# Kernel tuning notes

Hardware: AMD Instinct MI355X
Metric: run time of the kernel (lower is better)

## Reference

```python
import jax, jax.numpy as jnp
import numpy as np

D_MODEL = 1024
NUM_HEADS = 16
HEAD_DIM = D_MODEL // NUM_HEADS
B, S = 4, 2048


def setup_inputs() -> dict:
    key = jax.random.key(0)
    ks = jax.random.split(key, 12)
    s = 1.0 / np.sqrt(D_MODEL)
    return {
        "inputs_q": jax.random.normal(ks[0], (B, S, D_MODEL), jnp.float32),
        "inputs_k": jax.random.normal(ks[1], (B, S, D_MODEL), jnp.float32),
        "inputs_v": jax.random.normal(ks[2], (B, S, D_MODEL), jnp.float32),
        "Wq": jax.random.normal(ks[3], (D_MODEL, D_MODEL), jnp.float32) * s,
        "bq": jax.random.normal(ks[4], (D_MODEL,), jnp.float32) * 0.01,
        "Wk": jax.random.normal(ks[5], (D_MODEL, D_MODEL), jnp.float32) * s,
        "bk": jax.random.normal(ks[6], (D_MODEL,), jnp.float32) * 0.01,
        "Wv": jax.random.normal(ks[7], (D_MODEL, D_MODEL), jnp.float32) * s,
        "bv": jax.random.normal(ks[8], (D_MODEL,), jnp.float32) * 0.01,
        "Wo": jax.random.normal(ks[9], (D_MODEL, D_MODEL), jnp.float32) * s,
        "bo": jax.random.normal(ks[10], (D_MODEL,), jnp.float32) * 0.01,
    }


def reference(inputs_q, inputs_k, inputs_v, Wq, bq, Wk, bk, Wv, bv, Wo, bo):
    b, s, _ = inputs_q.shape
    # linear projections
    q = inputs_q @ Wq + bq  # [b, s, d_model]
    k = inputs_k @ Wk + bk
    v = inputs_v @ Wv + bv
    # split heads: bsd -> bhsd
    q = q.reshape(b, s, NUM_HEADS, HEAD_DIM).transpose(0, 2, 1, 3)
    k = k.reshape(b, s, NUM_HEADS, HEAD_DIM).transpose(0, 2, 1, 3)
    v = v.reshape(b, s, NUM_HEADS, HEAD_DIM).transpose(0, 2, 1, 3)
    scale = 1.0 / jnp.sqrt(jnp.asarray(HEAD_DIM, q.dtype))
    scores = jnp.einsum('bhqd,bhkd->bhqk', q, k) * scale  # [b,h,s,s]
    # causal mask: position q attends to k <= q
    causal = jnp.tril(jnp.ones((s, s), dtype=bool))
    scores = jnp.where(causal[None, None], scores, jnp.asarray(-jnp.inf, scores.dtype))
    attn = jax.nn.softmax(scores, axis=-1)
    ctx = jnp.einsum('bhqk,bhkd->bhqd', attn, v)  # [b,h,s,hd]
    ctx = ctx.transpose(0, 2, 1, 3).reshape(b, s, D_MODEL)
    return ctx @ Wo + bo
```

## Files before the change

kernel.cpp:

```cpp
#include <hip/hip_runtime.h>
#include <math.h>
#include <type_traits>

typedef __bf16 bf16;
typedef __attribute__((ext_vector_type(8))) __bf16 bf16x8;
typedef __attribute__((ext_vector_type(4))) float f32x4;
typedef __attribute__((ext_vector_type(16))) float f32x16;

#define SEQ 2048
#define DM 1024
#define NH 16
#define HD 64
#define BATCH 4

#define NEG_BIG (-1e30f)
#define SCALE_L2E 0.18033688011f

__device__ inline bf16x8 cvt_f32x8(const float* p) {
  f32x4 x0 = *(const f32x4*)p;
  f32x4 x1 = *(const f32x4*)(p + 4);
  bf16x8 r;
  r[0] = (bf16)x0[0]; r[1] = (bf16)x0[1]; r[2] = (bf16)x0[2]; r[3] = (bf16)x0[3];
  r[4] = (bf16)x1[0]; r[5] = (bf16)x1[1]; r[6] = (bf16)x1[2]; r[7] = (bf16)x1[3];
  return r;
}

__device__ inline void async_copy16(const bf16* g, bf16* l) {
  __builtin_amdgcn_global_load_lds(
      (const __attribute__((address_space(1))) unsigned int*)g,
      (__attribute__((address_space(3))) unsigned int*)l, 16, 0, 0);
}

__global__ __launch_bounds__(256) void cvt_kernel(const float* __restrict__ src,
                                                  bf16* __restrict__ dst) {
  size_t i = ((size_t)blockIdx.x * 256 + threadIdx.x) * 8;
  *(bf16x8*)(dst + i) = cvt_f32x8(src + i);
}

__global__ __launch_bounds__(256) void transpose_w_kernel(
    const float* __restrict__ Wq, const float* __restrict__ Wk,
    const float* __restrict__ Wv, const float* __restrict__ Wo,
    bf16* __restrict__ Tq, bf16* __restrict__ Tk,
    bf16* __restrict__ Tv, bf16* __restrict__ To) {
  __shared__ bf16 tile[64 * 66];
  int z = blockIdx.z;
  const float* src = (z == 0) ? Wq : (z == 1) ? Wk : (z == 2) ? Wv : Wo;
  bf16* dst = (z == 0) ? Tq : (z == 1) ? Tk : (z == 2) ? Tv : To;
  int n0 = blockIdx.x * 64, k0 = blockIdx.y * 64;
  int t = threadIdx.x;
  int c = t & 63, rr = t >> 6;
#pragma unroll
  for (int i = 0; i < 16; i++) {
    int k = i * 4 + rr;
    tile[k * 66 + c] = (bf16)src[(size_t)(k0 + k) * DM + n0 + c];
  }
  __syncthreads();
#pragma unroll
  for (int i = 0; i < 16; i++) {
    int n = i * 4 + rr;
    dst[(size_t)(n0 + n) * DM + k0 + c] = tile[c * 66 + n];
  }
}

__global__ __launch_bounds__(256) void transpose_v_kernel(
    const bf16* __restrict__ Vc, bf16* __restrict__ Vt) {
  __shared__ bf16 tile[64 * 66];
  int s0 = blockIdx.x * 64;
  int bh = blockIdx.y;
  int t = threadIdx.x;
  int c = t & 63, rr = t >> 6;
  const bf16* src = Vc + (size_t)bh * SEQ * HD;
  bf16* dst = Vt + (size_t)bh * HD * SEQ;
#pragma unroll
  for (int i = 0; i < 16; i++) {
    int s = i * 4 + rr;
    tile[s * 66 + c] = src[(size_t)(s0 + s) * HD + c];
  }
  __syncthreads();
#pragma unroll
  for (int i = 0; i < 16; i++) {
    int d = i * 4 + rr;
    dst[(size_t)d * SEQ + s0 + c] = tile[c * 66 + d];
  }
}

template <typename CT, int MODE>
__global__ __launch_bounds__(256) void gemm_bias_kernel(
    const bf16* __restrict__ A, const bf16* __restrict__ Bt,
    const float* __restrict__ bias, CT* __restrict__ C) {
  __shared__ bf16 As[128 * 32];
  __shared__ bf16 Bs[128 * 32];
  int m0 = blockIdx.x * 128, n0 = blockIdx.y * 128;
  int t = threadIdx.x;
  int wave = t >> 6, lane = t & 63, lr = lane & 15, lq = lane >> 4;
  int wm = (wave & 1) * 64, wn = (wave >> 1) * 64;

  f32x4 acc[4][4];
#pragma unroll
  for (int i = 0; i < 4; i++)
#pragma unroll
    for (int j = 0; j < 4; j++) acc[i][j] = (f32x4){0.f, 0.f, 0.f, 0.f};

  int srow = wave * 32 + (lane >> 2);
  int skc = lane & 3;
  const bf16* gA0 = A + (size_t)(m0 + srow) * DM + skc * 8;
  const bf16* gA1 = gA0 + (size_t)16 * DM;
  const bf16* gB0 = Bt + (size_t)(n0 + srow) * DM + skc * 8;
  const bf16* gB1 = gB0 + (size_t)16 * DM;
  bf16* lA0 = &As[(wave * 128) * 8];
  bf16* lA1 = &As[(wave * 128 + 64) * 8];
  bf16* lB0 = &Bs[(wave * 128) * 8];
  bf16* lB1 = &Bs[(wave * 128 + 64) * 8];

  for (int k0 = 0; k0 < DM; k0 += 32) {
    async_copy16(gA0, lA0);
    async_copy16(gA1, lA1);
    async_copy16(gB0, lB0);
    async_copy16(gB1, lB1);
    gA0 += 32; gA1 += 32; gB0 += 32; gB1 += 32;
    __syncthreads();

    bf16x8 af[4], bfr[4];
#pragma unroll
    for (int i = 0; i < 4; i++)
      af[i] = *(const bf16x8*)&As[(wm + i * 16 + lr) * 32 + lq * 8];
#pragma unroll
    for (int j = 0; j < 4; j++)
      bfr[j] = *(const bf16x8*)&Bs[(wn + j * 16 + lr) * 32 + lq * 8];
#pragma unroll
    for (int i = 0; i < 4; i++)
#pragma unroll
      for (int j = 0; j < 4; j++)
        acc[i][j] = __builtin_amdgcn_mfma_f32_16x16x32_bf16(af[i], bfr[j],
                                                            acc[i][j], 0, 0, 0);
    __syncthreads();
  }

#pragma unroll
  for (int j = 0; j < 4; j++) {
    int col = n0 + wn + j * 16 + lr;
    float bv = bias[col];
#pragma unroll
    for (int i = 0; i < 4; i++) {
      int row0 = m0 + wm + i * 16 + lq * 4;
#pragma unroll
      for (int r = 0; r < 4; r++) {
        int row = row0 + r;
        float v = acc[i][j][r] + bv;
        if constexpr (MODE == 0) {
          C[(size_t)row * DM + col] = (CT)v;
        } else {
          int b = row >> 11, s = row & 2047, h = col >> 6, d = col & 63;
          C[((size_t)(b * NH + h) * SEQ + s) * HD + d] = (CT)v;
        }
      }
    }
  }
}

__attribute__((amdgpu_waves_per_eu(4, 8)))
__global__ __launch_bounds__(256) void attention_kernel(
    const bf16* __restrict__ Qc, const bf16* __restrict__ Kc,
    const bf16* __restrict__ Vt, bf16* __restrict__ ctx) {
  __shared__ float ls_o[2][2][16][64];
  __shared__ float ls_ml[2][2][64];

  int t = threadIdx.x, wave = t >> 6, lane = t & 63;
  int l31 = lane & 31, hh = lane >> 5;
  int pair = wave >> 1, sub = wave & 1;

  int bid = blockIdx.x;
  int xcd = bid & 7, qq = bid >> 3;
  int g = xcd + 8 * (qq & 7);
  int bx = qq >> 3;
  int h = g & 15, b = g >> 4;

  int tq = pair ? (63 - bx) : bx;
  int q0 = tq * 32;
  int nch = tq + 1;
  int half = nch >> 1;
  int c0 = sub ? half : 0;
  int c1 = sub ? nch : half;

  const bf16* Qb = Qc + (size_t)(b * NH + h) * SEQ * HD;
  const bf16* Kb = Kc + (size_t)(b * NH + h) * SEQ * HD;
  const bf16* Vb = Vt + (size_t)(b * NH + h) * HD * SEQ;
  bf16* Cb = ctx + (size_t)b * SEQ * DM + h * HD;

  bf16x8 qf[4];
#pragma unroll
  for (int st = 0; st < 4; st++)
    qf[st] = *(const bf16x8*)&Qb[(size_t)(q0 + l31) * HD + st * 16 + hh * 8];

  f32x16 o[2];
#pragma unroll
  for (int dt = 0; dt < 2; dt++)
#pragma unroll
    for (int r = 0; r < 16; r++) o[dt][r] = 0.f;
  float m_st = NEG_BIG, l_st = 0.f;

#pragma unroll 1
  for (int c = c0; c < c1; c++) {
    int kv0 = c * 32;
    bf16x8 kf[4];
#pragma unroll
    for (int st = 0; st < 4; st++)
      kf[st] = *(const bf16x8*)&Kb[(size_t)(kv0 + l31) * HD + st * 16 + hh * 8];
    bf16x8 vf[2][2];
#pragma unroll
    for (int dt = 0; dt < 2; dt++)
#pragma unroll
      for (int ks = 0; ks < 2; ks++)
        vf[dt][ks] = *(const bf16x8*)&Vb[(size_t)(dt * 32 + l31) * SEQ + kv0 +
                                         ks * 16 + hh * 8];

    f32x16 s;
#pragma unroll
    for (int r = 0; r < 16; r++) s[r] = 0.f;
    __builtin_amdgcn_s_setprio(1);
#pragma unroll
    for (int st = 0; st < 4; st++)
      s = __builtin_amdgcn_mfma_f32_32x32x16_bf16(kf[st], qf[st], s, 0, 0, 0);
    __builtin_amdgcn_s_setprio(0);

    bool diag = (c == nch - 1);
    if (diag) {
      int q_g = q0 + l31;
#pragma unroll
      for (int r = 0; r < 16; r++) {
        int key = kv0 + (r & 3) + 8 * (r >> 2) + 4 * hh;
        float v = s[r] * SCALE_L2E;
        s[r] = (key > q_g) ? NEG_BIG : v;
      }
    } else {
#pragma unroll
      for (int r = 0; r < 16; r++) s[r] *= SCALE_L2E;
    }

    float mx = s[0];
#pragma unroll
    for (int r = 1; r < 16; r++) mx = fmaxf(mx, s[r]);
    mx = fmaxf(mx, __shfl_xor(mx, 32));
    float mnew = fmaxf(m_st, mx);
    float alpha = exp2f(m_st - mnew);
    m_st = mnew;
    float rs = 0.f;
#pragma unroll
    for (int r = 0; r < 16; r++) {
      float pv = exp2f(s[r] - mnew);
      s[r] = pv;
      rs += pv;
    }
    rs += __shfl_xor(rs, 32);
    l_st = l_st * alpha + rs;
#pragma unroll
    for (int dt = 0; dt < 2; dt++)
#pragma unroll
      for (int r = 0; r < 16; r++) o[dt][r] *= alpha;

    unsigned int W[8];
#pragma unroll
    for (int w = 0; w < 8; w++) {
      unsigned int u;
      asm("v_cvt_pk_bf16_f32 %0, %1, %2"
          : "=v"(u)
          : "v"(s[2 * w]), "v"(s[2 * w + 1]));
      W[w] = u;
    }
    bf16x8 pf[2];
    {
      unsigned int x1 = hh ? W[0] : W[2];
      unsigned int x2 = hh ? W[1] : W[3];
      unsigned int x3 = hh ? W[4] : W[6];
      unsigned int x4 = hh ? W[5] : W[7];
      unsigned int y1 = (unsigned int)__shfl_xor((int)x1, 32);
      unsigned int y2 = (unsigned int)__shfl_xor((int)x2, 32);
      unsigned int y3 = (unsigned int)__shfl_xor((int)x3, 32);
      unsigned int y4 = (unsigned int)__shfl_xor((int)x4, 32);
      unsigned int* f0 = (unsigned int*)&pf[0];
      unsigned int* f1 = (unsigned int*)&pf[1];
      f0[0] = hh ? y1 : W[0];
      f0[1] = hh ? y2 : W[1];
      f0[2] = hh ? W[2] : y1;
      f0[3] = hh ? W[3] : y2;
      f1[0] = hh ? y3 : W[4];
      f1[1] = hh ? y4 : W[5];
      f1[2] = hh ? W[6] : y3;
      f1[3] = hh ? W[7] : y4;
    }

    __builtin_amdgcn_s_setprio(1);
#pragma unroll
    for (int dt = 0; dt < 2; dt++)
#pragma unroll
      for (int ks = 0; ks < 2; ks++)
        o[dt] = __builtin_amdgcn_mfma_f32_32x32x16_bf16(vf[dt][ks], pf[ks],
                                                        o[dt], 0, 0, 0);
    __builtin_amdgcn_s_setprio(0);
  }

  if (sub) {
#pragma unroll
    for (int dt = 0; dt < 2; dt++)
#pragma unroll
      for (int r = 0; r < 16; r++) ls_o[pair][dt][r][lane] = o[dt][r];
    ls_ml[pair][0][lane] = m_st;
    ls_ml[pair][1][lane] = l_st;
  }
  __syncthreads();
  if (!sub) {
    float m2 = ls_ml[pair][0][lane], l2 = ls_ml[pair][1][lane];
    float m = fmaxf(m_st, m2);
    float a1 = exp2f(m_st - m), a2 = exp2f(m2 - m);
    float linv = 1.f / (l_st * a1 + l2 * a2);
    int row = q0 + l31;
#pragma unroll
    for (int dt = 0; dt < 2; dt++)
#pragma unroll
      for (int r = 0; r < 16; r += 2) {
        float va = (o[dt][r] * a1 + ls_o[pair][dt][r][lane] * a2) * linv;
        float vb =
            (o[dt][r + 1] * a1 + ls_o[pair][dt][r + 1][lane] * a2) * linv;
        unsigned int u;
        asm("v_cvt_pk_bf16_f32 %0, %1, %2" : "=v"(u) : "v"(va), "v"(vb));
        int d = dt * 32 + (r & 3) + 8 * (r >> 2) + 4 * hh;
        *(unsigned int*)&Cb[(size_t)row * DM + d] = u;
      }
  }
}

extern "C" void kernel_launch(void* const* d_in, const int* in_sizes, int n_in,
                              void* d_out, int out_size, void* d_ws,
                              size_t ws_size, hipStream_t stream) {
  const float* iq = (const float*)d_in[0];
  const float* ik = (const float*)d_in[1];
  const float* iv = (const float*)d_in[2];
  const float* Wq = (const float*)d_in[3];
  const float* bq = (const float*)d_in[4];
  const float* Wk = (const float*)d_in[5];
  const float* bk = (const float*)d_in[6];
  const float* Wv = (const float*)d_in[7];
  const float* bv = (const float*)d_in[8];
  const float* Wo = (const float*)d_in[9];
  const float* bo = (const float*)d_in[10];

  char* ws = (char*)d_ws;
  const size_t MB = 1024 * 1024;
  bf16* Tq = (bf16*)(ws + 0 * MB);
  bf16* Tk = (bf16*)(ws + 2 * MB);
  bf16* Tv = (bf16*)(ws + 4 * MB);
  bf16* To = (bf16*)(ws + 6 * MB);
  bf16* Qc = (bf16*)(ws + 8 * MB);
  bf16* Kc = (bf16*)(ws + 24 * MB);
  bf16* Vc = (bf16*)(ws + 40 * MB);
  bf16* X = (bf16*)d_out;
  bf16* Vtp = (bf16*)d_out;
  bf16* Cx = Vc;

  transpose_w_kernel<<<dim3(16, 16, 4), 256, 0, stream>>>(Wq, Wk, Wv, Wo, Tq,
                                                          Tk, Tv, To);
  cvt_kernel<<<dim3(4096), 256, 0, stream>>>(iq, X);
  gemm_bias_kernel<bf16, 1><<<dim3(64, 8), 256, 0, stream>>>(X, Tq, bq, Qc);
  cvt_kernel<<<dim3(4096), 256, 0, stream>>>(ik, X);
  gemm_bias_kernel<bf16, 1><<<dim3(64, 8), 256, 0, stream>>>(X, Tk, bk, Kc);
  cvt_kernel<<<dim3(4096), 256, 0, stream>>>(iv, X);
  gemm_bias_kernel<bf16, 1><<<dim3(64, 8), 256, 0, stream>>>(X, Tv, bv, Vc);
  transpose_v_kernel<<<dim3(32, 64), 256, 0, stream>>>(Vc, Vtp);
  attention_kernel<<<dim3(2048), 256, 0, stream>>>(Qc, Kc, Vtp, Cx);
  gemm_bias_kernel<float, 0><<<dim3(64, 8), 256, 0, stream>>>(Cx, To, bo,
                                                              (float*)d_out);
}
```

Baseline: 407.6 us.

## Fuse V transpose into projection epilogue and restructure attention work split

The V projection GEMM now writes its output directly in the transposed [b,h,d,s] layout, so the separate transpose kernel and its extra pass over memory go away. The attention kernel drops the split of KV chunks across wave pairs and the LDS merge that recombined them. Each wave now handles two query tiles (one short, one long) in sequence for causal balance, with double-buffered K/V register loads that overlap the next chunk's fetch with the current compute. In exchange, the grid shrinks from 2048 to 512 blocks, the waves_per_eu hint is removed, and the GEMM epilogue does strided stores into the transposed V layout.

```diff
diff --git a/kernel.cpp b/kernel.cpp
--- a/kernel.cpp
+++ b/kernel.cpp
@@ -62,28 +62,6 @@
   }
 }
 
-__global__ __launch_bounds__(256) void transpose_v_kernel(
-    const bf16* __restrict__ Vc, bf16* __restrict__ Vt) {
-  __shared__ bf16 tile[64 * 66];
-  int s0 = blockIdx.x * 64;
-  int bh = blockIdx.y;
-  int t = threadIdx.x;
-  int c = t & 63, rr = t >> 6;
-  const bf16* src = Vc + (size_t)bh * SEQ * HD;
-  bf16* dst = Vt + (size_t)bh * HD * SEQ;
-#pragma unroll
-  for (int i = 0; i < 16; i++) {
-    int s = i * 4 + rr;
-    tile[s * 66 + c] = src[(size_t)(s0 + s) * HD + c];
-  }
-  __syncthreads();
-#pragma unroll
-  for (int i = 0; i < 16; i++) {
-    int d = i * 4 + rr;
-    dst[(size_t)d * SEQ + s0 + c] = tile[c * 66 + d];
-  }
-}
-
 template <typename CT, int MODE>
 __global__ __launch_bounds__(256) void gemm_bias_kernel(
     const bf16* __restrict__ A, const bf16* __restrict__ Bt,
@@ -149,178 +127,174 @@
         float v = acc[i][j][r] + bv;
         if constexpr (MODE == 0) {
           C[(size_t)row * DM + col] = (CT)v;
+        } else if constexpr (MODE == 1) {
+          int b = row >> 11, s = row & 2047, h = col >> 6, d = col & 63;
+          C[((size_t)(b * NH + h) * SEQ + s) * HD + d] = (CT)v;
         } else {
           int b = row >> 11, s = row & 2047, h = col >> 6, d = col & 63;
-          C[((size_t)(b * NH + h) * SEQ + s) * HD + d] = (CT)v;
+          C[((size_t)(b * NH + h) * HD + d) * SEQ + s] = (CT)v;
         }
       }
     }
   }
 }
 
-__attribute__((amdgpu_waves_per_eu(4, 8)))
 __global__ __launch_bounds__(256) void attention_kernel(
     const bf16* __restrict__ Qc, const bf16* __restrict__ Kc,
     const bf16* __restrict__ Vt, bf16* __restrict__ ctx) {
-  __shared__ float ls_o[2][2][16][64];
-  __shared__ float ls_ml[2][2][64];
-
   int t = threadIdx.x, wave = t >> 6, lane = t & 63;
   int l31 = lane & 31, hh = lane >> 5;
-  int pair = wave >> 1, sub = wave & 1;
 
   int bid = blockIdx.x;
   int xcd = bid & 7, qq = bid >> 3;
   int g = xcd + 8 * (qq & 7);
   int bx = qq >> 3;
   int h = g & 15, b = g >> 4;
-
-  int tq = pair ? (63 - bx) : bx;
-  int q0 = tq * 32;
-  int nch = tq + 1;
-  int half = nch >> 1;
-  int c0 = sub ? half : 0;
-  int c1 = sub ? nch : half;
+  int p = bx * 4 + wave;
 
   const bf16* Qb = Qc + (size_t)(b * NH + h) * SEQ * HD;
   const bf16* Kb = Kc + (size_t)(b * NH + h) * SEQ * HD;
   const bf16* Vb = Vt + (size_t)(b * NH + h) * HD * SEQ;
   bf16* Cb = ctx + (size_t)b * SEQ * DM + h * HD;
 
-  bf16x8 qf[4];
-#pragma unroll
-  for (int st = 0; st < 4; st++)
-    qf[st] = *(const bf16x8*)&Qb[(size_t)(q0 + l31) * HD + st * 16 + hh * 8];
-
-  f32x16 o[2];
-#pragma unroll
-  for (int dt = 0; dt < 2; dt++)
-#pragma unroll
-    for (int r = 0; r < 16; r++) o[dt][r] = 0.f;
-  float m_st = NEG_BIG, l_st = 0.f;
-
 #pragma unroll 1
-  for (int c = c0; c < c1; c++) {
-    int kv0 = c * 32;
-    bf16x8 kf[4];
+  for (int pass = 0; pass < 2; pass++) {
+    int tq = pass ? (63 - p) : p;
+    int q0 = tq * 32;
+    int nch = tq + 1;
+    int nch_ev = (nch + 1) & ~1;
+
+    bf16x8 qf[4];
 #pragma unroll
     for (int st = 0; st < 4; st++)
-      kf[st] = *(const bf16x8*)&Kb[(size_t)(kv0 + l31) * HD + st * 16 + hh * 8];
-    bf16x8 vf[2][2];
+      qf[st] = *(const bf16x8*)&Qb[(size_t)(q0 + l31) * HD + st * 16 + hh * 8];
+
+    f32x16 o[2];
 #pragma unroll
     for (int dt = 0; dt < 2; dt++)
 #pragma unroll
-      for (int ks = 0; ks < 2; ks++)
-        vf[dt][ks] = *(const bf16x8*)&Vb[(size_t)(dt * 32 + l31) * SEQ + kv0 +
-                                         ks * 16 + hh * 8];
-
-    f32x16 s;
-#pragma unroll
-    for (int r = 0; r < 16; r++) s[r] = 0.f;
-    __builtin_amdgcn_s_setprio(1);
-#pragma unroll
-    for (int st = 0; st < 4; st++)
-      s = __builtin_amdgcn_mfma_f32_32x32x16_bf16(kf[st], qf[st], s, 0, 0, 0);
-    __builtin_amdgcn_s_setprio(0);
-
-    bool diag = (c == nch - 1);
-    if (diag) {
-      int q_g = q0 + l31;
+      for (int r = 0; r < 16; r++) o[dt][r] = 0.f;
+    float m_st = NEG_BIG, l_st = 0.f;
+
+    bf16x8 kfA[4], vfA[2][2], kfB[4], vfB[2][2];
+
+    auto loadkv = [&](bf16x8(&kf)[4], bf16x8(&vf)[2][2], int c) {
+      int kv0 = c * 32;
+#pragma unroll
+      for (int st = 0; st < 4; st++)
+        kf[st] =
+            *(const bf16x8*)&Kb[(size_t)(kv0 + l31) * HD + st * 16 + hh * 8];
+#pragma unroll
+      for (int dt = 0; dt < 2; dt++)
+#pragma unroll
+        for (int ks = 0; ks < 2; ks++)
+          vf[dt][ks] = *(const bf16x8*)&Vb[(size_t)(dt * 32 + l31) * SEQ + kv0 +
+                                           ks * 16 + hh * 8];
+    };
+
+    auto compute = [&](bf16x8(&kf)[4], bf16x8(&vf)[2][2], int c) {
+      int kv0 = c * 32;
+      f32x16 s;
+#pragma unroll
+      for (int r = 0; r < 16; r++) s[r] = 0.f;
+      __builtin_amdgcn_s_setprio(1);
+#pragma unroll
+      for (int st = 0; st < 4; st++)
+        s = __builtin_amdgcn_mfma_f32_32x32x16_bf16(kf[st], qf[st], s, 0, 0, 0);
+      __builtin_amdgcn_s_setprio(0);
+
+      if (c >= nch - 1) {
+        int q_g = q0 + l31;
+#pragma unroll
+        for (int r = 0; r < 16; r++) {
+          int key = kv0 + (r & 3) + 8 * (r >> 2) + 4 * hh;
+          float v = s[r] * SCALE_L2E;
+          s[r] = (key > q_g) ? NEG_BIG : v;
+        }
+      } else {
+#pragma unroll
+        for (int r = 0; r < 16; r++) s[r] *= SCALE_L2E;
+      }
+
+      float mx = s[0];
+#pragma unroll
+      for (int r = 1; r < 16; r++) mx = fmaxf(mx, s[r]);
+      mx = fmaxf(mx, __shfl_xor(mx, 32));
+      float mnew = fmaxf(m_st, mx);
+      float alpha = exp2f(m_st - mnew);
+      m_st = mnew;
+      float rs = 0.f;
 #pragma unroll
       for (int r = 0; r < 16; r++) {
-        int key = kv0 + (r & 3) + 8 * (r >> 2) + 4 * hh;
-        float v = s[r] * SCALE_L2E;
-        s[r] = (key > q_g) ? NEG_BIG : v;
-      }
-    } else {
-#pragma unroll
-      for (int r = 0; r < 16; r++) s[r] *= SCALE_L2E;
+        float pv = exp2f(s[r] - mnew);
+        s[r] = pv;
+        rs += pv;
+      }
+      rs += __shfl_xor(rs, 32);
+      l_st = l_st * alpha + rs;
+#pragma unroll
+      for (int dt = 0; dt < 2; dt++)
+#pragma unroll
+        for (int r = 0; r < 16; r++) o[dt][r] *= alpha;
+
+      unsigned int W[8];
+#pragma unroll
+      for (int w = 0; w < 8; w++) {
+        unsigned int u;
+        asm("v_cvt_pk_bf16_f32 %0, %1, %2"
+            : "=v"(u)
+            : "v"(s[2 * w]), "v"(s[2 * w + 1]));
+        W[w] = u;
+      }
+      bf16x8 pf[2];
+      {
+        unsigned int x1 = hh ? W[0] : W[2];
+        unsigned int x2 = hh ? W[1] : W[3];
+        unsigned int x3 = hh ? W[4] : W[6];
+        unsigned int x4 = hh ? W[5] : W[7];
+        unsigned int y1 = (unsigned int)__shfl_xor((int)x1, 32);
+        unsigned int y2 = (unsigned int)__shfl_xor((int)x2, 32);
+        unsigned int y3 = (unsigned int)__shfl_xor((int)x3, 32);
+        unsigned int y4 = (unsigned int)__shfl_xor((int)x4, 32);
+        unsigned int* f0 = (unsigned int*)&pf[0];
+        unsigned int* f1 = (unsigned int*)&pf[1];
+        f0[0] = hh ? y1 : W[0];
+        f0[1] = hh ? y2 : W[1];
+        f0[2] = hh ? W[2] : y1;
+        f0[3] = hh ? W[3] : y2;
+        f1[0] = hh ? y3 : W[4];
+        f1[1] = hh ? y4 : W[5];
+        f1[2] = hh ? W[6] : y3;
+        f1[3] = hh ? W[7] : y4;
+      }
+
+      __builtin_amdgcn_s_setprio(1);
+#pragma unroll
+      for (int dt = 0; dt < 2; dt++)
+#pragma unroll
+        for (int ks = 0; ks < 2; ks++)
+          o[dt] = __builtin_amdgcn_mfma_f32_32x32x16_bf16(vf[dt][ks], pf[ks],
+                                                          o[dt], 0, 0, 0);
+      __builtin_amdgcn_s_setprio(0);
+    };
+
+    loadkv(kfA, vfA, 0);
+#pragma unroll 1
+    for (int c = 0; c < nch_ev; c += 2) {
+      loadkv(kfB, vfB, c + 1);
+      compute(kfA, vfA, c);
+      if (c + 2 < nch_ev) loadkv(kfA, vfA, c + 2);
+      compute(kfB, vfB, c + 1);
     }
 
-    float mx = s[0];
-#pragma unroll
-    for (int r = 1; r < 16; r++) mx = fmaxf(mx, s[r]);
-    mx = fmaxf(mx, __shfl_xor(mx, 32));
-    float mnew = fmaxf(m_st, mx);
-    float alpha = exp2f(m_st - mnew);
-    m_st = mnew;
-    float rs = 0.f;
-#pragma unroll
-    for (int r = 0; r < 16; r++) {
-      float pv = exp2f(s[r] - mnew);
-      s[r] = pv;
-      rs += pv;
-    }
-    rs += __shfl_xor(rs, 32);
-    l_st = l_st * alpha + rs;
+    float inv = 1.f / l_st;
+    int row = q0 + l31;
 #pragma unroll
     for (int dt = 0; dt < 2; dt++)
 #pragma unroll
-      for (int r = 0; r < 16; r++) o[dt][r] *= alpha;
-
-    unsigned int W[8];
-#pragma unroll
-    for (int w = 0; w < 8; w++) {
-      unsigned int u;
-      asm("v_cvt_pk_bf16_f32 %0, %1, %2"
-          : "=v"(u)
-          : "v"(s[2 * w]), "v"(s[2 * w + 1]));
-      W[w] = u;
-    }
-    bf16x8 pf[2];
-    {
-      unsigned int x1 = hh ? W[0] : W[2];
-      unsigned int x2 = hh ? W[1] : W[3];
-      unsigned int x3 = hh ? W[4] : W[6];
-      unsigned int x4 = hh ? W[5] : W[7];
-      unsigned int y1 = (unsigned int)__shfl_xor((int)x1, 32);
-      unsigned int y2 = (unsigned int)__shfl_xor((int)x2, 32);
-      unsigned int y3 = (unsigned int)__shfl_xor((int)x3, 32);
-      unsigned int y4 = (unsigned int)__shfl_xor((int)x4, 32);
-      unsigned int* f0 = (unsigned int*)&pf[0];
-      unsigned int* f1 = (unsigned int*)&pf[1];
-      f0[0] = hh ? y1 : W[0];
-      f0[1] = hh ? y2 : W[1];
-      f0[2] = hh ? W[2] : y1;
-      f0[3] = hh ? W[3] : y2;
-      f1[0] = hh ? y3 : W[4];
-      f1[1] = hh ? y4 : W[5];
-      f1[2] = hh ? W[6] : y3;
-      f1[3] = hh ? W[7] : y4;
-    }
-
-    __builtin_amdgcn_s_setprio(1);
-#pragma unroll
-    for (int dt = 0; dt < 2; dt++)
-#pragma unroll
-      for (int ks = 0; ks < 2; ks++)
-        o[dt] = __builtin_amdgcn_mfma_f32_32x32x16_bf16(vf[dt][ks], pf[ks],
-                                                        o[dt], 0, 0, 0);
-    __builtin_amdgcn_s_setprio(0);
-  }
-
-  if (sub) {
-#pragma unroll
-    for (int dt = 0; dt < 2; dt++)
-#pragma unroll
-      for (int r = 0; r < 16; r++) ls_o[pair][dt][r][lane] = o[dt][r];
-    ls_ml[pair][0][lane] = m_st;
-    ls_ml[pair][1][lane] = l_st;
-  }
-  __syncthreads();
-  if (!sub) {
-    float m2 = ls_ml[pair][0][lane], l2 = ls_ml[pair][1][lane];
-    float m = fmaxf(m_st, m2);
-    float a1 = exp2f(m_st - m), a2 = exp2f(m2 - m);
-    float linv = 1.f / (l_st * a1 + l2 * a2);
-    int row = q0 + l31;
-#pragma unroll
-    for (int dt = 0; dt < 2; dt++)
-#pragma unroll
       for (int r = 0; r < 16; r += 2) {
-        float va = (o[dt][r] * a1 + ls_o[pair][dt][r][lane] * a2) * linv;
-        float vb =
-            (o[dt][r + 1] * a1 + ls_o[pair][dt][r + 1][lane] * a2) * linv;
+        float va = o[dt][r] * inv;
+        float vb = o[dt][r + 1] * inv;
         unsigned int u;
         asm("v_cvt_pk_bf16_f32 %0, %1, %2" : "=v"(u) : "v"(va), "v"(vb));
         int d = dt * 32 + (r & 3) + 8 * (r >> 2) + 4 * hh;
@@ -352,10 +326,9 @@
   bf16* To = (bf16*)(ws + 6 * MB);
   bf16* Qc = (bf16*)(ws + 8 * MB);
   bf16* Kc = (bf16*)(ws + 24 * MB);
-  bf16* Vc = (bf16*)(ws + 40 * MB);
-  bf16* X = (bf16*)d_out;
+  bf16* X = (bf16*)(ws + 40 * MB);
   bf16* Vtp = (bf16*)d_out;
-  bf16* Cx = Vc;
+  bf16* Cx = (bf16*)(ws + 40 * MB);
 
   transpose_w_kernel<<<dim3(16, 16, 4), 256, 0, stream>>>(Wq, Wk, Wv, Wo, Tq,
                                                           Tk, Tv, To);
@@ -364,9 +337,8 @@
   cvt_kernel<<<dim3(4096), 256, 0, stream>>>(ik, X);
   gemm_bias_kernel<bf16, 1><<<dim3(64, 8), 256, 0, stream>>>(X, Tk, bk, Kc);
   cvt_kernel<<<dim3(4096), 256, 0, stream>>>(iv, X);
-  gemm_bias_kernel<bf16, 1><<<dim3(64, 8), 256, 0, stream>>>(X, Tv, bv, Vc);
-  transpose_v_kernel<<<dim3(32, 64), 256, 0, stream>>>(Vc, Vtp);
-  attention_kernel<<<dim3(2048), 256, 0, stream>>>(Qc, Kc, Vtp, Cx);
+  gemm_bias_kernel<bf16, 2><<<dim3(64, 8), 256, 0, stream>>>(X, Tv, bv, Vtp);
+  attention_kernel<<<dim3(512), 256, 0, stream>>>(Qc, Kc, Vtp, Cx);
   gemm_bias_kernel<float, 0><<<dim3(64, 8), 256, 0, stream>>>(Cx, To, bo,
                                                               (float*)d_out);
 }
```

After: 403.4 us. About the same (-1.0%).
